# Kernel tuning notes

Measured on AMD Instinct MI355X. Metric: run time of the kernel, lower is better.

The kernel has to match this reference:

```python
import jax, jax.numpy as jnp
import numpy as np
import math

NUM_HEADS = 16
N_WIRES = 8  # == d_k


def setup_inputs() -> dict:
    key = jax.random.key(0)
    k1, k2, k3, k4 = jax.random.split(key, 4)
    B, S, E = 4, 2048, NUM_HEADS * N_WIRES
    x = jax.random.normal(k1, (B, S, E), dtype=jnp.float32)
    theta = jax.random.normal(k2, (N_WIRES,), dtype=jnp.float32)
    W_combine = jax.random.normal(k3, (E, E), dtype=jnp.float32) * (1.0 / math.sqrt(E))
    b_combine = jax.random.normal(k4, (E,), dtype=jnp.float32) * 0.01
    return {"x": x, "theta": theta, "W_combine": W_combine, "b_combine": b_combine}


def _quantum_heads(x, theta, H, dk):
    # since single-qubit RX gates compose and the state stays a product state.
    B, S, E = x.shape
    proj = x.reshape(B, S, H, dk)  # [B,S,H,dk]
    return jnp.cos(proj + theta)   # theta broadcasts over wires (dk == n_wires)


def reference(x, theta, W_combine, b_combine):
    B, S, E = x.shape
    H, dk = NUM_HEADS, N_WIRES
    qkv = _quantum_heads(x, theta, H, dk)          # [B,S,H,dk]; q = k = v
    qh = jnp.transpose(qkv, (0, 2, 1, 3))           # [B,H,S,dk]
    scores = jnp.einsum('bhqd,bhkd->bhqk', qh, qh) / math.sqrt(dk)
    attn = jax.nn.softmax(scores, axis=-1)          # [B,H,S,S]
    out = jnp.einsum('bhqk,bhkd->bhqd', attn, qh)   # [B,H,S,dk]
    out = jnp.transpose(out, (0, 2, 1, 3)).reshape(B, S, E)
    return out @ W_combine.T + b_combine
```

## Files before the change

kernel.cpp:

```cpp
#include <hip/hip_runtime.h>

typedef _Float16 f16;
typedef _Float16 f16x2 __attribute__((ext_vector_type(2)));
typedef _Float16 f16x4 __attribute__((ext_vector_type(4)));
typedef float    f32x4 __attribute__((ext_vector_type(4)));
typedef unsigned int u32;
typedef unsigned int u32x2v __attribute__((ext_vector_type(2)));

#define NS 2048
#define NH 16
#define NDK 8
#define NE 128
#define CHUNK 512
#define NCHUNK 4
#define CSCALE 0.51006972f

__device__ __forceinline__ float fexp2(float v){
#if __has_builtin(__builtin_amdgcn_exp2f)
  return __builtin_amdgcn_exp2f(v);
#else
  return exp2f(v);
#endif
}

__device__ __forceinline__ f16x2 pkrtz(float a, float b){
  return __builtin_bit_cast(f16x2, __builtin_amdgcn_cvt_pkrtz(a, b));
}

__device__ __forceinline__ float fdot2a(f16x2 a, f16x2 b, float c){
#if __has_builtin(__builtin_amdgcn_fdot2)
  return __builtin_amdgcn_fdot2(a, b, c, false);
#else
  return c + (float)a[0]*(float)b[0] + (float)a[1]*(float)b[1];
#endif
}

#define GLOAD16(g, l) __builtin_amdgcn_global_load_lds( \
    (const __attribute__((address_space(1))) u32*)(g), \
    (__attribute__((address_space(3))) u32*)(l), 16, 0, 0)

__global__ __launch_bounds__(256) void qcos(const float* __restrict__ x,
                                            const float* __restrict__ theta,
                                            u32* __restrict__ kbuf,
                                            u32* __restrict__ vbuf){
  __shared__ __align__(16) uint4 Lt[16*17];
  const int bid = blockIdx.x;
  const int b   = bid >> 7;
  const int t   = bid & 127;
  const int tid = threadIdx.x;

  const float4 thA = ((const float4*)theta)[0];
  const float4 thB = ((const float4*)theta)[1];

  {
    const int sl = tid & 15, h = tid >> 4;
    const int s  = t*16 + sl;
    const float* xp = x + ((size_t)(b*NS + s)*NE + h*NDK);
    const float4 x0 = ((const float4*)xp)[0];
    const float4 x1 = ((const float4*)xp)[1];
    union { f16 hh[8]; uint4 u; } pk;
    pk.hh[0] = (f16)__cosf(x0.x + thA.x);
    pk.hh[1] = (f16)__cosf(x0.y + thA.y);
    pk.hh[2] = (f16)__cosf(x0.z + thA.z);
    pk.hh[3] = (f16)__cosf(x0.w + thA.w);
    pk.hh[4] = (f16)__cosf(x1.x + thB.x);
    pk.hh[5] = (f16)__cosf(x1.y + thB.y);
    pk.hh[6] = (f16)__cosf(x1.z + thB.z);
    pk.hh[7] = (f16)__cosf(x1.w + thB.w);
    ((uint4*)kbuf)[(size_t)(b*16 + h)*NS + s] = pk.u;
    Lt[h*17 + sl] = pk.u;
  }
  __syncthreads();

  {
    const int h  = tid >> 4;
    const int d  = (tid >> 1) & 7;
    const int gp = tid & 1;
    const unsigned short* Ls = (const unsigned short*)Lt;
    union { unsigned short us[8]; uint4 u; } pk;
    #pragma unroll
    for(int j = 0; j < 8; ++j)
      pk.us[j] = Ls[(h*17 + 8*gp + j)*8 + d];
    ((uint4*)vbuf)[((size_t)(b*16 + h)*128 + t)*16 + d*2 + gp] = pk.u;
  }
}

#define QTILE(T, VPO, KPO, ACC) do{ \
    uint2 ka_ = (KPO)[(T)*32]; \
    uint2 va_ = (VPO)[(T)*32]; \
    f16x4 kf_ = __builtin_bit_cast(f16x4, ka_); \
    f16x4 vf_ = __builtin_bit_cast(f16x4, va_); \
    f32x4 st_ = __builtin_amdgcn_mfma_f32_16x16x16f16(kf_, qf, z4, 0, 0, 0); \
    f16x2 plo_ = pkrtz(fexp2(st_[0]), fexp2(st_[1])); \
    f16x2 phi_ = pkrtz(fexp2(st_[2]), fexp2(st_[3])); \
    u32x2v pu_ = { __builtin_bit_cast(u32, plo_), __builtin_bit_cast(u32, phi_) }; \
    f16x4 pf_ = __builtin_bit_cast(f16x4, pu_); \
    ACC = __builtin_amdgcn_mfma_f32_16x16x16f16(vf_, pf_, ACC, 0, 0, 0); \
  }while(0)

__global__ __launch_bounds__(512, 4) void qattn(const u32* __restrict__ kbuf,
                                                const u32* __restrict__ vbuf,
                                                float* __restrict__ out){
  __shared__ __align__(16) u32 Kc[2][2048];
  __shared__ __align__(16) u32 Vt[2][2048];
  __shared__ __align__(16) u32 OnesR[512];

  const int bid  = blockIdx.x;
  const int bh   = bid >> 4;
  const int qc   = bid & 15;
  const int tid  = threadIdx.x;
  const int lane = tid & 63;
  const int w    = tid >> 6;
  const int c    = lane & 15;
  const int grp  = lane >> 4;
  const int g1   = grp & 1;
  const bool lo32  = lane < 32;
  const bool creal = c < 8;

  const u32* kb = kbuf + (size_t)bh*8192;
  const u32* vb = vbuf + (size_t)bh*8192;

  OnesR[tid] = 0x3C003C00u;

  const u32* gk = kb + (size_t)tid*4;
  const u32* gv = vb + (size_t)tid*4;

  const int qrow = qc*128 + w*16 + c;
  uint2 qv = make_uint2(0u, 0u);
  if(lo32) qv = *(const uint2*)(kb + (size_t)qrow*4 + g1*2);
  f16x4 q4 = __builtin_bit_cast(f16x4, qv);
  q4 *= (f16)CSCALE;
  const f16x4 qf = q4;

  const u32 vlane = ((u32)(c & 7))*32u + ((u32)grp)*8u;
  const char* onesc = (const char*)OnesR;

  const f32x4 z4 = {0.f, 0.f, 0.f, 0.f};
  f32x4 acc0 = z4, acc1 = z4;

  GLOAD16(gk, &Kc[0][w*256]);
  GLOAD16(gv, &Vt[0][w*256]);

  for(int cc = 0; cc < NCHUNK; ++cc){
    __syncthreads();
    if(cc + 1 < NCHUNK){
      GLOAD16(gk + (size_t)(cc+1)*2048, &Kc[(cc+1)&1][w*256]);
      GLOAD16(gv + (size_t)(cc+1)*2048, &Vt[(cc+1)&1][w*256]);
    }
    const uint2* kp = (const uint2*)&Kc[cc&1][0] + c*2 + g1;
    const char*  vc = (const char*)&Vt[cc&1][0] + vlane;
    #pragma unroll
    for(int o = 0; o < 4; ++o){
      const uint2* kpo = kp + o*256;
      const uint2* vpo = (const uint2*)(creal ? vc + o*2048 : onesc);
      QTILE(0, vpo, kpo, acc0);
      QTILE(1, vpo, kpo, acc1);
      QTILE(2, vpo, kpo, acc0);
      QTILE(3, vpo, kpo, acc1);
      QTILE(4, vpo, kpo, acc0);
      QTILE(5, vpo, kpo, acc1);
      QTILE(6, vpo, kpo, acc0);
      QTILE(7, vpo, kpo, acc1);
    }
  }

  f32x4 accT;
  accT[0] = acc0[0]+acc1[0]; accT[1] = acc0[1]+acc1[1];
  accT[2] = acc0[2]+acc1[2]; accT[3] = acc0[3]+acc1[3];
  const int b = bh >> 4, h = bh & 15;
  float den = __shfl(accT[0], 32 + c, 64);
  if(lo32){
    float inv = 1.0f / den;
    float4 o;
    o.x = accT[0]*inv; o.y = accT[1]*inv; o.z = accT[2]*inv; o.w = accT[3]*inv;
    *(float4*)(out + ((size_t)(b*NS + qrow)*NH + h)*NDK + grp*4) = o;
  }
}

__global__ __launch_bounds__(256) void qcomb(const float* __restrict__ W,
                                             const float* __restrict__ bias,
                                             float* __restrict__ io){
  __shared__ __align__(16) u32 Wt[64*132];
  __shared__ __align__(16) u32 A2[32*65];
  const int tid = threadIdx.x;
  const size_t row0 = (size_t)blockIdx.x * 32;

  #pragma unroll
  for(int i=0;i<32;++i){
    int g = tid + 256*i;
    int j = g >> 6, e2 = g & 63;
    const float* wp = W + (size_t)j*NE + 2*e2;
    f16x2 wv = pkrtz(wp[0], wp[1]);
    Wt[e2*132 + j] = __builtin_bit_cast(u32, wv);
  }
  #pragma unroll
  for(int i=0;i<8;++i){
    int g = tid + 256*i;
    int r = g >> 6, e2 = g & 63;
    const float* ap = io + (row0 + r)*NE + 2*e2;
    f16x2 av = pkrtz(ap[0], ap[1]);
    A2[r*65 + e2] = __builtin_bit_cast(u32, av);
  }
  __syncthreads();

  const int tr = tid >> 4, tc = tid & 15;
  float acc0[8] = {0,0,0,0,0,0,0,0};
  float acc1[8] = {0,0,0,0,0,0,0,0};
  for(int e2=0; e2<64; ++e2){
    f16x2 a0 = __builtin_bit_cast(f16x2, A2[tr*65 + e2]);
    f16x2 a1 = __builtin_bit_cast(f16x2, A2[(tr+16)*65 + e2]);
    const u32* wr = &Wt[e2*132 + tc*8];
    #pragma unroll
    for(int cj=0; cj<8; ++cj){
      f16x2 wv = __builtin_bit_cast(f16x2, wr[cj]);
      acc0[cj] = fdot2a(a0, wv, acc0[cj]);
      acc1[cj] = fdot2a(a1, wv, acc1[cj]);
    }
  }

  float4 b0 = *(const float4*)(bias + tc*8);
  float4 b1 = *(const float4*)(bias + tc*8 + 4);
  float* o0 = io + (row0 + tr)*NE + tc*8;
  float* o1 = io + (row0 + tr + 16)*NE + tc*8;
  float4 v;
  v.x = acc0[0]+b0.x; v.y = acc0[1]+b0.y; v.z = acc0[2]+b0.z; v.w = acc0[3]+b0.w;
  *(float4*)(o0) = v;
  v.x = acc0[4]+b1.x; v.y = acc0[5]+b1.y; v.z = acc0[6]+b1.z; v.w = acc0[7]+b1.w;
  *(float4*)(o0+4) = v;
  v.x = acc1[0]+b0.x; v.y = acc1[1]+b0.y; v.z = acc1[2]+b0.z; v.w = acc1[3]+b0.w;
  *(float4*)(o1) = v;
  v.x = acc1[4]+b1.x; v.y = acc1[5]+b1.y; v.z = acc1[6]+b1.z; v.w = acc1[7]+b1.w;
  *(float4*)(o1+4) = v;
}

extern "C" void kernel_launch(void* const* d_in, const int* in_sizes, int n_in,
                              void* d_out, int out_size, void* d_ws, size_t ws_size,
                              hipStream_t stream) {
  (void)in_sizes; (void)n_in; (void)out_size; (void)ws_size;
  const float* x     = (const float*)d_in[0];
  const float* theta = (const float*)d_in[1];
  const float* W     = (const float*)d_in[2];
  const float* bias  = (const float*)d_in[3];
  float* out = (float*)d_out;
  u32* kbuf = (u32*)d_ws;
  u32* vbuf = kbuf + 524288;

  qcos <<<512, 256, 0, stream>>>(x, theta, kbuf, vbuf);
  qattn<<<1024, 512, 0, stream>>>(kbuf, vbuf, out);
  qcomb<<<256, 256, 0, stream>>>(W, bias, out);
}
```

Before: 53.70 us.

## Process two query tiles per wave to reuse K/V LDS loads, halve grid

Each wave now handles 32 query rows, two 16-row MFMA tiles, instead of 16, so every K and V fragment read from LDS feeds two score and two PV MFMAs. The grid shrinks from 1024 to 512 blocks, halving the total K/V global-to-LDS traffic. The ones-row for the softmax denominator now comes from a per-lane select instead of an LDS buffer. In exchange there are more live registers, more ILP per wave, and fewer blocks to fill the GPU.

```diff
diff --git a/kernel.cpp b/kernel.cpp
--- a/kernel.cpp
+++ b/kernel.cpp
@@ -14,6 +14,7 @@
 #define CHUNK 512
 #define NCHUNK 4
 #define CSCALE 0.51006972f
+#define ONE2 0x3C003C00u
 
 __device__ __forceinline__ float fexp2(float v){
 #if __has_builtin(__builtin_amdgcn_exp2f)
@@ -85,17 +86,24 @@
   }
 }
 
-#define QTILE(T, VPO, KPO, ACC) do{ \
+#define QTILE(T, VPO, KPO, ACCA, ACCB) do{ \
     uint2 ka_ = (KPO)[(T)*32]; \
     uint2 va_ = (VPO)[(T)*32]; \
+    u32 w0_ = creal ? va_.x : ONE2; \
+    u32 w1_ = creal ? va_.y : ONE2; \
+    u32x2v vu_ = { w0_, w1_ }; \
     f16x4 kf_ = __builtin_bit_cast(f16x4, ka_); \
-    f16x4 vf_ = __builtin_bit_cast(f16x4, va_); \
-    f32x4 st_ = __builtin_amdgcn_mfma_f32_16x16x16f16(kf_, qf, z4, 0, 0, 0); \
-    f16x2 plo_ = pkrtz(fexp2(st_[0]), fexp2(st_[1])); \
-    f16x2 phi_ = pkrtz(fexp2(st_[2]), fexp2(st_[3])); \
-    u32x2v pu_ = { __builtin_bit_cast(u32, plo_), __builtin_bit_cast(u32, phi_) }; \
-    f16x4 pf_ = __builtin_bit_cast(f16x4, pu_); \
-    ACC = __builtin_amdgcn_mfma_f32_16x16x16f16(vf_, pf_, ACC, 0, 0, 0); \
+    f16x4 vf_ = __builtin_bit_cast(f16x4, vu_); \
+    f32x4 s0_ = __builtin_amdgcn_mfma_f32_16x16x16f16(kf_, qf0, z4, 0, 0, 0); \
+    f32x4 s1_ = __builtin_amdgcn_mfma_f32_16x16x16f16(kf_, qf1, z4, 0, 0, 0); \
+    f16x2 a0_ = pkrtz(fexp2(s0_[0]), fexp2(s0_[1])); \
+    f16x2 b0_ = pkrtz(fexp2(s0_[2]), fexp2(s0_[3])); \
+    f16x2 a1_ = pkrtz(fexp2(s1_[0]), fexp2(s1_[1])); \
+    f16x2 b1_ = pkrtz(fexp2(s1_[2]), fexp2(s1_[3])); \
+    u32x2v p0_ = { __builtin_bit_cast(u32, a0_), __builtin_bit_cast(u32, b0_) }; \
+    u32x2v p1_ = { __builtin_bit_cast(u32, a1_), __builtin_bit_cast(u32, b1_) }; \
+    ACCA = __builtin_amdgcn_mfma_f32_16x16x16f16(vf_, __builtin_bit_cast(f16x4, p0_), ACCA, 0, 0, 0); \
+    ACCB = __builtin_amdgcn_mfma_f32_16x16x16f16(vf_, __builtin_bit_cast(f16x4, p1_), ACCB, 0, 0, 0); \
   }while(0)
 
 __global__ __launch_bounds__(512, 4) void qattn(const u32* __restrict__ kbuf,
@@ -103,11 +111,10 @@
                                                 float* __restrict__ out){
   __shared__ __align__(16) u32 Kc[2][2048];
   __shared__ __align__(16) u32 Vt[2][2048];
-  __shared__ __align__(16) u32 OnesR[512];
 
   const int bid  = blockIdx.x;
-  const int bh   = bid >> 4;
-  const int qc   = bid & 15;
+  const int bh   = bid >> 3;
+  const int qc   = bid & 7;
   const int tid  = threadIdx.x;
   const int lane = tid & 63;
   const int w    = tid >> 6;
@@ -120,23 +127,27 @@
   const u32* kb = kbuf + (size_t)bh*8192;
   const u32* vb = vbuf + (size_t)bh*8192;
 
-  OnesR[tid] = 0x3C003C00u;
-
   const u32* gk = kb + (size_t)tid*4;
   const u32* gv = vb + (size_t)tid*4;
 
-  const int qrow = qc*128 + w*16 + c;
-  uint2 qv = make_uint2(0u, 0u);
-  if(lo32) qv = *(const uint2*)(kb + (size_t)qrow*4 + g1*2);
-  f16x4 q4 = __builtin_bit_cast(f16x4, qv);
-  q4 *= (f16)CSCALE;
-  const f16x4 qf = q4;
+  const int qrow0 = qc*256 + w*32 + c;
+  const int qrow1 = qrow0 + 16;
+  uint2 qv0 = make_uint2(0u, 0u), qv1 = make_uint2(0u, 0u);
+  if(lo32){
+    qv0 = *(const uint2*)(kb + (size_t)qrow0*4 + g1*2);
+    qv1 = *(const uint2*)(kb + (size_t)qrow1*4 + g1*2);
+  }
+  f16x4 q40 = __builtin_bit_cast(f16x4, qv0);
+  f16x4 q41 = __builtin_bit_cast(f16x4, qv1);
+  q40 *= (f16)CSCALE;
+  q41 *= (f16)CSCALE;
+  const f16x4 qf0 = q40, qf1 = q41;
 
   const u32 vlane = ((u32)(c & 7))*32u + ((u32)grp)*8u;
-  const char* onesc = (const char*)OnesR;
 
   const f32x4 z4 = {0.f, 0.f, 0.f, 0.f};
-  f32x4 acc0 = z4, acc1 = z4;
+  f32x4 accA0 = z4, accB0 = z4;
+  f32x4 accA1 = z4, accB1 = z4;
 
   GLOAD16(gk, &Kc[0][w*256]);
   GLOAD16(gv, &Vt[0][w*256]);
@@ -148,32 +159,46 @@
       GLOAD16(gv + (size_t)(cc+1)*2048, &Vt[(cc+1)&1][w*256]);
     }
     const uint2* kp = (const uint2*)&Kc[cc&1][0] + c*2 + g1;
-    const char*  vc = (const char*)&Vt[cc&1][0] + vlane;
+    const uint2* vp = (const uint2*)((const char*)&Vt[cc&1][0] + vlane);
     #pragma unroll
     for(int o = 0; o < 4; ++o){
       const uint2* kpo = kp + o*256;
-      const uint2* vpo = (const uint2*)(creal ? vc + o*2048 : onesc);
-      QTILE(0, vpo, kpo, acc0);
-      QTILE(1, vpo, kpo, acc1);
-      QTILE(2, vpo, kpo, acc0);
-      QTILE(3, vpo, kpo, acc1);
-      QTILE(4, vpo, kpo, acc0);
-      QTILE(5, vpo, kpo, acc1);
-      QTILE(6, vpo, kpo, acc0);
-      QTILE(7, vpo, kpo, acc1);
-    }
-  }
-
-  f32x4 accT;
-  accT[0] = acc0[0]+acc1[0]; accT[1] = acc0[1]+acc1[1];
-  accT[2] = acc0[2]+acc1[2]; accT[3] = acc0[3]+acc1[3];
+      const uint2* vpo = vp + o*256;
+      QTILE(0, vpo, kpo, accA0, accA1);
+      QTILE(1, vpo, kpo, accB0, accB1);
+      QTILE(2, vpo, kpo, accA0, accA1);
+      QTILE(3, vpo, kpo, accB0, accB1);
+      QTILE(4, vpo, kpo, accA0, accA1);
+      QTILE(5, vpo, kpo, accB0, accB1);
+      QTILE(6, vpo, kpo, accA0, accA1);
+      QTILE(7, vpo, kpo, accB0, accB1);
+    }
+  }
+
   const int b = bh >> 4, h = bh & 15;
-  float den = __shfl(accT[0], 32 + c, 64);
-  if(lo32){
-    float inv = 1.0f / den;
-    float4 o;
-    o.x = accT[0]*inv; o.y = accT[1]*inv; o.z = accT[2]*inv; o.w = accT[3]*inv;
-    *(float4*)(out + ((size_t)(b*NS + qrow)*NH + h)*NDK + grp*4) = o;
+  {
+    f32x4 aT;
+    aT[0]=accA0[0]+accB0[0]; aT[1]=accA0[1]+accB0[1];
+    aT[2]=accA0[2]+accB0[2]; aT[3]=accA0[3]+accB0[3];
+    float den = __shfl(aT[0], 32 + c, 64);
+    if(lo32){
+      float inv = 1.0f / den;
+      float4 o;
+      o.x = aT[0]*inv; o.y = aT[1]*inv; o.z = aT[2]*inv; o.w = aT[3]*inv;
+      *(float4*)(out + ((size_t)(b*NS + qrow0)*NH + h)*NDK + grp*4) = o;
+    }
+  }
+  {
+    f32x4 aT;
+    aT[0]=accA1[0]+accB1[0]; aT[1]=accA1[1]+accB1[1];
+    aT[2]=accA1[2]+accB1[2]; aT[3]=accA1[3]+accB1[3];
+    float den = __shfl(aT[0], 32 + c, 64);
+    if(lo32){
+      float inv = 1.0f / den;
+      float4 o;
+      o.x = aT[0]*inv; o.y = aT[1]*inv; o.z = aT[2]*inv; o.w = aT[3]*inv;
+      *(float4*)(out + ((size_t)(b*NS + qrow1)*NH + h)*NDK + grp*4) = o;
+    }
   }
 }
 
@@ -246,6 +271,6 @@
   u32* vbuf = kbuf + 524288;
 
   qcos <<<512, 256, 0, stream>>>(x, theta, kbuf, vbuf);
-  qattn<<<1024, 512, 0, stream>>>(kbuf, vbuf, out);
+  qattn<<<512, 512, 0, stream>>>(kbuf, vbuf, out);
   qcomb<<<256, 256, 0, stream>>>(W, bias, out);
 }
```

Result: faster. 51.05 us (-4.9%).
